# Performance work log

Hardware: AMD Instinct MI355X
Metric: run time of the kernel (lower is better)

## Reference

```python
import jax, jax.numpy as jnp
import numpy as np

B, NPG, E, D, H = 64, 4096, 4194304, 384, 32
N = B * NPG

def setup_inputs() -> dict:
    key = jax.random.key(0)
    ks = jax.random.split(key, 10)
    x = jax.random.normal(ks[0], (N, D), jnp.float32)
    edge_index = jax.random.randint(ks[1], (2, E), 0, N, dtype=jnp.int32)
    batch = jnp.repeat(jnp.arange(B, dtype=jnp.int32), NPG)
    s = 0.05
    W1 = jax.random.normal(ks[2], (D, H), jnp.float32) * s
    b1 = jnp.zeros((H,), jnp.float32)
    W2 = jax.random.normal(ks[3], (H, 8), jnp.float32) * s
    b2 = jnp.zeros((8,), jnp.float32)
    W3 = jax.random.normal(ks[4], (8, 8), jnp.float32) * s
    b3 = jnp.zeros((8,), jnp.float32)
    W4 = jax.random.normal(ks[5], (8, 2), jnp.float32) * s
    b4 = jnp.zeros((2,), jnp.float32)
    return {"x": x, "edge_index": edge_index, "batch": batch,
            "W1": W1, "b1": b1, "W2": W2, "b2": b2,
            "W3": W3, "b3": b3, "W4": W4, "b4": b4}

def _leaky(v):
    return jnp.where(v > 0, v, 0.2 * v)

def reference(x, edge_index, batch, W1, b1, W2, b2, W3, b3, W4, b4):
    n = x.shape[0]
    loop = jnp.arange(n, dtype=edge_index.dtype)
    src = jnp.concatenate([edge_index[0], loop])  # [E+N]
    dst = jnp.concatenate([edge_index[1], loop])
    # GCN symmetric normalization with self-loops (edge_weight = 1)
    deg = jax.ops.segment_sum(jnp.ones(src.shape[0], jnp.float32), dst, num_segments=n)
    dis = jnp.where(deg > 0, jax.lax.rsqrt(jnp.maximum(deg, 1.0)), 0.0)
    norm = (dis[src] * dis[dst])[:, None]  # [E+N, 1]

    def gcn(h, W, b):
        h = h @ W                                   # project first (PyG order)
        agg = jax.ops.segment_sum(h[src] * norm, dst, num_segments=n)
        return agg + b

    h = _leaky(gcn(x, W1, b1))   # [N, 32]
    h = _leaky(gcn(h, W2, b2))   # [N, 8]
    bs = int(np.asarray(batch).max()) + 1
    g = jnp.mean(h.reshape(bs, -1, h.shape[-1]), axis=1)  # mean readout [B, 8]
    g = _leaky(g @ W3 + b3)      # lin1 + leaky_relu; dropout is identity (eval)
    return g @ W4 + b4           # [B, 2]
```

## Files before the change

### kernel.cpp

```cpp
#include <hip/hip_runtime.h>
#include <cstdint>

__device__ __forceinline__ float leaky(float v) { return v > 0.f ? v : 0.2f * v; }


#define NPB 512

__global__ __launch_bounds__(256) void k_bin1(const int* __restrict__ dst,
                                              int* __restrict__ counts,
                                              int E, int CHUNK, int NBKT, int NBLK1) {
  __shared__ int hist[NPB];
  int t = threadIdx.x;
  int blk = blockIdx.x;
  for (int i = t; i < NBKT; i += 256) hist[i] = 0;
  __syncthreads();
  int e0 = blk * CHUNK;
  int e1 = min(e0 + CHUNK, E);
  for (int e = e0 + t; e < e1; e += 256) atomicAdd(&hist[dst[e] >> 9], 1);
  __syncthreads();
  for (int i = t; i < NBKT; i += 256) counts[i * NBLK1 + blk] = hist[i];
}

__global__ __launch_bounds__(256) void k_scan1(const int* __restrict__ cnt,
                                               int* __restrict__ bsums) {
  __shared__ int red[256];
  int t = threadIdx.x;
  int base = blockIdx.x * 1024;
  int s = cnt[base + t] + cnt[base + t + 256] + cnt[base + t + 512] + cnt[base + t + 768];
  red[t] = s;
  __syncthreads();
  for (int off = 128; off > 0; off >>= 1) {
    if (t < off) red[t] += red[t + off];
    __syncthreads();
  }
  if (t == 0) bsums[blockIdx.x] = red[0];
}

__global__ __launch_bounds__(256) void k_scan2(int* __restrict__ bsums, int* __restrict__ S,
                                               int total, int E, int nb) {
  __shared__ int sc[256];
  int t = threadIdx.x;
  int v = (t < nb) ? bsums[t] : 0;
  sc[t] = v;
  __syncthreads();
  for (int off = 1; off < 256; off <<= 1) {
    int u = (t >= off) ? sc[t - off] : 0;
    __syncthreads();
    sc[t] += u;
    __syncthreads();
  }
  if (t < nb) bsums[t] = (t == 0) ? 0 : sc[t - 1];
  if (t == 0) S[total] = E;
}

__global__ __launch_bounds__(256) void k_scan3(const int* __restrict__ cnt,
                                               const int* __restrict__ bsums,
                                               int* __restrict__ S) {
  __shared__ int sc[256];
  int t = threadIdx.x;
  int base = blockIdx.x * 1024;
  int4 d = *(const int4*)(cnt + base + 4 * t);
  int tot = d.x + d.y + d.z + d.w;
  sc[t] = tot;
  __syncthreads();
  for (int off = 1; off < 256; off <<= 1) {
    int u = (t >= off) ? sc[t - off] : 0;
    __syncthreads();
    sc[t] += u;
    __syncthreads();
  }
  int toff = bsums[blockIdx.x] + ((t == 0) ? 0 : sc[t - 1]);
  int4 ro;
  ro.x = toff;
  ro.y = toff + d.x;
  ro.z = toff + d.x + d.y;
  ro.w = toff + d.x + d.y + d.z;
  *(int4*)(S + base + 4 * t) = ro;
}

__global__ __launch_bounds__(256) void k_bin2(const int* __restrict__ ei,
                                              const int* __restrict__ S,
                                              int2* __restrict__ binned,
                                              int E, int CHUNK, int NBKT, int NBLK1) {
  __shared__ int cur[NPB];
  int t = threadIdx.x;
  int blk = blockIdx.x;
  for (int i = t; i < NBKT; i += 256) cur[i] = S[i * NBLK1 + blk];
  __syncthreads();
  int e0 = blk * CHUNK;
  int e1 = min(e0 + CHUNK, E);
  for (int e = e0 + t; e < e1; e += 256) {
    int s = ei[e];
    int d = ei[E + e];
    int pos = atomicAdd(&cur[d >> 9], 1);
    binned[pos] = make_int2(s, d);
  }
}

__global__ __launch_bounds__(256) void k_build(const int2* __restrict__ binned,
                                               const int* __restrict__ S,
                                               int* __restrict__ row_off,
                                               float* __restrict__ dis,
                                               int* __restrict__ csr,
                                               int E, int N, int NBKT, int NBLK1) {
  __shared__ int h[NPB];
  __shared__ int cur[NPB];
  int t = threadIdx.x;
  int b = blockIdx.x;
  int node0 = b * NPB;
  int begb = S[b * NBLK1];
  int endb = (b + 1 < NBKT) ? S[(b + 1) * NBLK1] : E;
  for (int i = t; i < NPB; i += 256) h[i] = 0;
  __syncthreads();
  for (int e = begb + t; e < endb; e += 256) atomicAdd(&h[binned[e].y - node0], 1);
  __syncthreads();
  for (int off = 1; off < NPB; off <<= 1) {
    int i0 = t, i1 = t + 256;
    int a0 = (i0 >= off) ? h[i0 - off] : 0;
    int a1 = (i1 >= off) ? h[i1 - off] : 0;
    __syncthreads();
    h[i0] += a0;
    h[i1] += a1;
    __syncthreads();
  }
  for (int i = t; i < NPB; i += 256) {
    int incl = h[i];
    int excl = i ? h[i - 1] : 0;
    row_off[node0 + i] = begb + excl;
    cur[i] = excl;
    dis[node0 + i] = rsqrtf((float)(incl - excl + 1));
  }
  __syncthreads();
  for (int e = begb + t; e < endb; e += 256) {
    int2 ed = binned[e];
    int pos = atomicAdd(&cur[ed.y - node0], 1);
    csr[begb + pos] = ed.x;
  }
  if (b == NBKT - 1 && t == 0) row_off[N] = E;
}


__global__ __launch_bounds__(256) void k_gemm1(const float* __restrict__ x,
                                               const float* __restrict__ W1,
                                               float* __restrict__ h1) {
  __shared__ float xl[32 * 256];
  __shared__ float wl[32 * 32];
  int t = threadIdx.x;
  size_t n0 = (size_t)blockIdx.x * 256;
  int fg8 = (t & 3) * 8;
  int ng4 = (t >> 2) * 4;
  float acc[4][8];
#pragma unroll
  for (int i = 0; i < 4; i++)
#pragma unroll
    for (int c = 0; c < 8; c++) acc[i][c] = 0.f;

  for (int kc = 0; kc < 384; kc += 32) {
    __syncthreads();
#pragma unroll
    for (int g = 0; g < 2; g++) {
      float4 v[4];
#pragma unroll
      for (int i = 0; i < 4; i++) {
        int idx = g * 1024 + i * 256 + t;
        int k4 = idx & 7;
        int n = idx >> 3;
        v[i] = *(const float4*)(x + (n0 + n) * 384 + kc + k4 * 4);
      }
#pragma unroll
      for (int i = 0; i < 4; i++) {
        int idx = g * 1024 + i * 256 + t;
        int k4 = idx & 7;
        int n = idx >> 3;
        xl[(k4 * 4 + 0) * 256 + n] = v[i].x;
        xl[(k4 * 4 + 1) * 256 + n] = v[i].y;
        xl[(k4 * 4 + 2) * 256 + n] = v[i].z;
        xl[(k4 * 4 + 3) * 256 + n] = v[i].w;
      }
    }
    ((float4*)wl)[t] = ((const float4*)(W1 + kc * 32))[t];
    __syncthreads();
#pragma unroll
    for (int k = 0; k < 32; k++) {
      float4 xv = *(const float4*)&xl[k * 256 + ng4];
      float4 wa = *(const float4*)&wl[k * 32 + fg8];
      float4 wb = *(const float4*)&wl[k * 32 + fg8 + 4];
      float xr[4] = {xv.x, xv.y, xv.z, xv.w};
      float wr[8] = {wa.x, wa.y, wa.z, wa.w, wb.x, wb.y, wb.z, wb.w};
#pragma unroll
      for (int i = 0; i < 4; i++)
#pragma unroll
        for (int c = 0; c < 8; c++) acc[i][c] = fmaf(xr[i], wr[c], acc[i][c]);
    }
  }
#pragma unroll
  for (int i = 0; i < 4; i++) {
    float* dst = h1 + (n0 + ng4 + i) * 32 + fg8;
    *(float4*)dst = make_float4(acc[i][0], acc[i][1], acc[i][2], acc[i][3]);
    *((float4*)dst + 1) = make_float4(acc[i][4], acc[i][5], acc[i][6], acc[i][7]);
  }
}


__global__ __launch_bounds__(256) void k_agg1_fused(const float* __restrict__ h1,
                                                    const float* __restrict__ dis,
                                                    const int* __restrict__ row_off,
                                                    const int* __restrict__ csr,
                                                    const float* __restrict__ b1,
                                                    const float* __restrict__ W2,
                                                    float* __restrict__ h2) {
  __shared__ float w2s[256];
  int t = threadIdx.x;
  w2s[t] = W2[t];
  __syncthreads();
  int lane = t & 63;
  int half = lane >> 5;
  int j = lane & 31;
  int n = blockIdx.x * 4 + (t >> 6);
  int beg = row_off[n], end = row_off[n + 1];
  float dn = dis[n];
  float acc = half ? 0.f : h1[(size_t)n * 32 + j] * dn;
  int p = beg + half;
  for (; p + 2 < end; p += 4) {
    int s0 = csr[p], s1 = csr[p + 2];
    float d0 = dis[s0], d1 = dis[s1];
    float v0 = h1[(size_t)s0 * 32 + j];
    float v1 = h1[(size_t)s1 * 32 + j];
    acc += v0 * d0 + v1 * d1;
  }
  if (p < end) {
    int s = csr[p];
    acc += h1[(size_t)s * 32 + j] * dis[s];
  }
  acc += __shfl_xor(acc, 32);
  float o = leaky(acc * dn + b1[j]);
  float pr[8];
#pragma unroll
  for (int c = 0; c < 8; c++) pr[c] = o * w2s[j * 8 + c];
#pragma unroll
  for (int off = 1; off < 32; off <<= 1) {
#pragma unroll
    for (int c = 0; c < 8; c++) pr[c] += __shfl_xor(pr[c], off);
  }
  if (j == 0) {
    float4 v = half ? make_float4(pr[4], pr[5], pr[6], pr[7])
                    : make_float4(pr[0], pr[1], pr[2], pr[3]);
    *(float4*)(h2 + (size_t)n * 8 + half * 4) = v;
  }
}


__global__ __launch_bounds__(256) void k_agg2(const float* __restrict__ h2,
                                              const float* __restrict__ dis,
                                              const int* __restrict__ row_off,
                                              const int* __restrict__ csr,
                                              const float* __restrict__ b2,
                                              float* __restrict__ out2) {
  int t = threadIdx.x;
  int j = t & 7;
  int sub = (t >> 3) & 1;
  int n = blockIdx.x * 16 + (t >> 4);
  int beg = row_off[n], end = row_off[n + 1];
  float dn = dis[n];
  float acc = sub ? 0.f : h2[(size_t)n * 8 + j] * dn;
  int p = beg + sub;
  for (; p + 2 < end; p += 4) {
    int s0 = csr[p], s1 = csr[p + 2];
    float d0 = dis[s0], d1 = dis[s1];
    acc += h2[(size_t)s0 * 8 + j] * d0 + h2[(size_t)s1 * 8 + j] * d1;
  }
  if (p < end) {
    int s = csr[p];
    acc += h2[(size_t)s * 8 + j] * dis[s];
  }
  acc += __shfl_xor(acc, 8);
  if (!sub) out2[(size_t)n * 8 + j] = leaky(acc * dn + b2[j]);
}


__global__ __launch_bounds__(256) void k_readout(const float* __restrict__ out2,
                                                 float* __restrict__ g, int NPG) {
  __shared__ float red[256];
  int t = threadIdx.x;
  int j = t & 7, r0 = t >> 3;
  const float* base = out2 + (size_t)blockIdx.x * NPG * 8;
  float s = 0.f;
  for (int r = r0; r < NPG; r += 32) s += base[(size_t)r * 8 + j];
  red[t] = s;
  __syncthreads();
  if (t < 8) {
    float tot = 0.f;
    for (int q = 0; q < 32; q++) tot += red[t + 8 * q];
    g[blockIdx.x * 8 + t] = tot / (float)NPG;
  }
}


__global__ __launch_bounds__(64) void k_mlp(const float* __restrict__ g,
                                            const float* __restrict__ W3,
                                            const float* __restrict__ b3,
                                            const float* __restrict__ W4,
                                            const float* __restrict__ b4,
                                            float* __restrict__ out, int B) {
  int b = threadIdx.x;
  if (b >= B) return;
  float gi[8], t1[8];
#pragma unroll
  for (int k = 0; k < 8; k++) gi[k] = g[b * 8 + k];
#pragma unroll
  for (int jj = 0; jj < 8; jj++) {
    float s = b3[jj];
#pragma unroll
    for (int k = 0; k < 8; k++) s = fmaf(gi[k], W3[k * 8 + jj], s);
    t1[jj] = leaky(s);
  }
#pragma unroll
  for (int jj = 0; jj < 2; jj++) {
    float s = b4[jj];
#pragma unroll
    for (int k = 0; k < 8; k++) s = fmaf(t1[k], W4[k * 2 + jj], s);
    out[b * 2 + jj] = s;
  }
}

extern "C" void kernel_launch(void* const* d_in, const int* in_sizes, int n_in,
                              void* d_out, int out_size, void* d_ws, size_t ws_size,
                              hipStream_t stream) {
  const float* x  = (const float*)d_in[0];
  const int*   ei = (const int*)d_in[1];
  const float* W1 = (const float*)d_in[3];
  const float* b1 = (const float*)d_in[4];
  const float* W2 = (const float*)d_in[5];
  const float* b2 = (const float*)d_in[6];
  const float* W3 = (const float*)d_in[7];
  const float* b3 = (const float*)d_in[8];
  const float* W4 = (const float*)d_in[9];
  const float* b4 = (const float*)d_in[10];

  const int E = in_sizes[1] / 2;
  const int N = in_sizes[2];
  const int B = out_size / 2;
  const int NPG = N / B;

  const int NBKT  = N / NPB;
  const int NBLK1 = 512;
  const int CHUNK = (E + NBLK1 - 1) / NBLK1;
  const int SCN   = NBKT * NBLK1;
  const int NBS   = SCN / 1024;

  size_t off = 0;
  auto place = [&](size_t bytes) {
    size_t p = off;
    off = (off + bytes + 255) & ~(size_t)255;
    return p;
  };
  size_t o_counts  = place((size_t)SCN * 4);
  size_t o_S       = place(((size_t)SCN + 1) * 4);
  size_t o_bsums   = place(1024 * 4);
  size_t o_dis     = place((size_t)N * 4);
  size_t o_row_off = place(((size_t)N + 1) * 4);
  size_t o_csr     = place((size_t)E * 4);
  size_t o_binned  = place((size_t)E * 8);
  size_t o_h2      = place((size_t)N * 8 * 4);
  size_t o_gbuf    = place((size_t)B * 8 * 4);
  if (off > ws_size || N % NPB != 0) {
    hipMemsetAsync(d_out, 0, (size_t)out_size * 4, stream);
    return;
  }
  char* ws = (char*)d_ws;
  int*   counts  = (int*)(ws + o_counts);
  int*   S       = (int*)(ws + o_S);
  int*   bsums   = (int*)(ws + o_bsums);
  float* dis     = (float*)(ws + o_dis);
  int*   row_off = (int*)(ws + o_row_off);
  int*   csr     = (int*)(ws + o_csr);
  int2*  binned  = (int2*)(ws + o_binned);
  float* h1      = (float*)(ws + o_binned);
  float* h2      = (float*)(ws + o_h2);
  float* gbuf    = (float*)(ws + o_gbuf);
  float* out2    = h1;

  k_bin1<<<NBLK1, 256, 0, stream>>>(ei + E, counts, E, CHUNK, NBKT, NBLK1);
  k_scan1<<<NBS, 256, 0, stream>>>(counts, bsums);
  k_scan2<<<1, 256, 0, stream>>>(bsums, S, SCN, E, NBS);
  k_scan3<<<NBS, 256, 0, stream>>>(counts, bsums, S);
  k_bin2<<<NBLK1, 256, 0, stream>>>(ei, S, binned, E, CHUNK, NBKT, NBLK1);
  k_build<<<NBKT, 256, 0, stream>>>(binned, S, row_off, dis, csr, E, N, NBKT, NBLK1);
  k_gemm1<<<N / 256, 256, 0, stream>>>(x, W1, h1);
  k_agg1_fused<<<N / 4, 256, 0, stream>>>(h1, dis, row_off, csr, b1, W2, h2);
  k_agg2<<<N / 16, 256, 0, stream>>>(h2, dis, row_off, csr, b2, out2);
  k_readout<<<B, 256, 0, stream>>>(out2, gbuf, NPG);
  k_mlp<<<1, 64, 0, stream>>>(gbuf, W3, b3, W4, b4, (float*)d_out, B);
}
```

Baseline: 0.9997 ms.

## Store features in bf16, pack binned edges, fuse readout into agg2

Intermediate node features h1 and h2 are now stored as bf16 instead of fp32, which halves the bytes moved by the random gathers in both aggregation passes. Binned edges are packed into one int (source shifted left by 9, with the destination's low 9 bits) instead of an int2, which halves binning traffic. The gather loops are unrolled to four neighbours per step, and the mean readout is fused into the second aggregation through per-block atomics on a zeroed buffer. The costs are lower precision in the intermediates, packed source ids that overflow past 2^22 nodes, and floating-point atomics that make the sum order nondeterministic.

Measured after the change: 966.9 us. -3.3%, faster.

```diff
diff --git a/kernel.cpp b/kernel.cpp
--- a/kernel.cpp
+++ b/kernel.cpp
@@ -2,7 +2,14 @@
 #include <cstdint>
 
 __device__ __forceinline__ float leaky(float v) { return v > 0.f ? v : 0.2f * v; }
-
+__device__ __forceinline__ unsigned short f2bf(float f) {
+  unsigned int u = __float_as_uint(f);
+  unsigned int r = (u + 0x7FFFu + ((u >> 16) & 1u)) >> 16;
+  return (unsigned short)r;
+}
+__device__ __forceinline__ float bf2f(unsigned short h) {
+  return __uint_as_float(((unsigned int)h) << 16);
+}
 
 #define NPB 512
 
@@ -80,7 +87,7 @@
 
 __global__ __launch_bounds__(256) void k_bin2(const int* __restrict__ ei,
                                               const int* __restrict__ S,
-                                              int2* __restrict__ binned,
+                                              int* __restrict__ binned,
                                               int E, int CHUNK, int NBKT, int NBLK1) {
   __shared__ int cur[NPB];
   int t = threadIdx.x;
@@ -93,11 +100,11 @@
     int s = ei[e];
     int d = ei[E + e];
     int pos = atomicAdd(&cur[d >> 9], 1);
-    binned[pos] = make_int2(s, d);
-  }
-}
-
-__global__ __launch_bounds__(256) void k_build(const int2* __restrict__ binned,
+    binned[pos] = (s << 9) | (d & 511);
+  }
+}
+
+__global__ __launch_bounds__(256) void k_build(const int* __restrict__ binned,
                                                const int* __restrict__ S,
                                                int* __restrict__ row_off,
                                                float* __restrict__ dis,
@@ -112,7 +119,7 @@
   int endb = (b + 1 < NBKT) ? S[(b + 1) * NBLK1] : E;
   for (int i = t; i < NPB; i += 256) h[i] = 0;
   __syncthreads();
-  for (int e = begb + t; e < endb; e += 256) atomicAdd(&h[binned[e].y - node0], 1);
+  for (int e = begb + t; e < endb; e += 256) atomicAdd(&h[binned[e] & 511], 1);
   __syncthreads();
   for (int off = 1; off < NPB; off <<= 1) {
     int i0 = t, i1 = t + 256;
@@ -132,9 +139,9 @@
   }
   __syncthreads();
   for (int e = begb + t; e < endb; e += 256) {
-    int2 ed = binned[e];
-    int pos = atomicAdd(&cur[ed.y - node0], 1);
-    csr[begb + pos] = ed.x;
+    int ed = binned[e];
+    int pos = atomicAdd(&cur[ed & 511], 1);
+    csr[begb + pos] = ed >> 9;
   }
   if (b == NBKT - 1 && t == 0) row_off[N] = E;
 }
@@ -142,7 +149,7 @@
 
 __global__ __launch_bounds__(256) void k_gemm1(const float* __restrict__ x,
                                                const float* __restrict__ W1,
-                                               float* __restrict__ h1) {
+                                               unsigned short* __restrict__ h1b) {
   __shared__ float xl[32 * 256];
   __shared__ float wl[32 * 32];
   int t = threadIdx.x;
@@ -195,20 +202,23 @@
   }
 #pragma unroll
   for (int i = 0; i < 4; i++) {
-    float* dst = h1 + (n0 + ng4 + i) * 32 + fg8;
-    *(float4*)dst = make_float4(acc[i][0], acc[i][1], acc[i][2], acc[i][3]);
-    *((float4*)dst + 1) = make_float4(acc[i][4], acc[i][5], acc[i][6], acc[i][7]);
-  }
-}
-
-
-__global__ __launch_bounds__(256) void k_agg1_fused(const float* __restrict__ h1,
+    uint4 pk;
+    pk.x = (unsigned)f2bf(acc[i][0]) | ((unsigned)f2bf(acc[i][1]) << 16);
+    pk.y = (unsigned)f2bf(acc[i][2]) | ((unsigned)f2bf(acc[i][3]) << 16);
+    pk.z = (unsigned)f2bf(acc[i][4]) | ((unsigned)f2bf(acc[i][5]) << 16);
+    pk.w = (unsigned)f2bf(acc[i][6]) | ((unsigned)f2bf(acc[i][7]) << 16);
+    *(uint4*)(h1b + (n0 + ng4 + i) * 32 + fg8) = pk;
+  }
+}
+
+
+__global__ __launch_bounds__(256) void k_agg1_fused(const unsigned short* __restrict__ h1b,
                                                     const float* __restrict__ dis,
                                                     const int* __restrict__ row_off,
                                                     const int* __restrict__ csr,
                                                     const float* __restrict__ b1,
                                                     const float* __restrict__ W2,
-                                                    float* __restrict__ h2) {
+                                                    unsigned short* __restrict__ h2b) {
   __shared__ float w2s[256];
   int t = threadIdx.x;
   w2s[t] = W2[t];
@@ -219,18 +229,20 @@
   int n = blockIdx.x * 4 + (t >> 6);
   int beg = row_off[n], end = row_off[n + 1];
   float dn = dis[n];
-  float acc = half ? 0.f : h1[(size_t)n * 32 + j] * dn;
+  float acc = half ? 0.f : bf2f(h1b[(size_t)n * 32 + j]) * dn;
   int p = beg + half;
-  for (; p + 2 < end; p += 4) {
-    int s0 = csr[p], s1 = csr[p + 2];
-    float d0 = dis[s0], d1 = dis[s1];
-    float v0 = h1[(size_t)s0 * 32 + j];
-    float v1 = h1[(size_t)s1 * 32 + j];
-    acc += v0 * d0 + v1 * d1;
-  }
-  if (p < end) {
+  for (; p + 6 < end; p += 8) {
+    int s0 = csr[p], s1 = csr[p + 2], s2 = csr[p + 4], s3 = csr[p + 6];
+    float d0 = dis[s0], d1 = dis[s1], d2 = dis[s2], d3 = dis[s3];
+    float v0 = bf2f(h1b[(size_t)s0 * 32 + j]);
+    float v1 = bf2f(h1b[(size_t)s1 * 32 + j]);
+    float v2 = bf2f(h1b[(size_t)s2 * 32 + j]);
+    float v3 = bf2f(h1b[(size_t)s3 * 32 + j]);
+    acc += v0 * d0 + v1 * d1 + v2 * d2 + v3 * d3;
+  }
+  for (; p < end; p += 2) {
     int s = csr[p];
-    acc += h1[(size_t)s * 32 + j] * dis[s];
+    acc += bf2f(h1b[(size_t)s * 32 + j]) * dis[s];
   }
   acc += __shfl_xor(acc, 32);
   float o = leaky(acc * dn + b1[j]);
@@ -242,56 +254,55 @@
 #pragma unroll
     for (int c = 0; c < 8; c++) pr[c] += __shfl_xor(pr[c], off);
   }
-  if (j == 0) {
-    float4 v = half ? make_float4(pr[4], pr[5], pr[6], pr[7])
-                    : make_float4(pr[0], pr[1], pr[2], pr[3]);
-    *(float4*)(h2 + (size_t)n * 8 + half * 4) = v;
-  }
-}
-
-
-__global__ __launch_bounds__(256) void k_agg2(const float* __restrict__ h2,
-                                              const float* __restrict__ dis,
-                                              const int* __restrict__ row_off,
-                                              const int* __restrict__ csr,
-                                              const float* __restrict__ b2,
-                                              float* __restrict__ out2) {
+  if (lane == 0) {
+    uint4 pk;
+    pk.x = (unsigned)f2bf(pr[0]) | ((unsigned)f2bf(pr[1]) << 16);
+    pk.y = (unsigned)f2bf(pr[2]) | ((unsigned)f2bf(pr[3]) << 16);
+    pk.z = (unsigned)f2bf(pr[4]) | ((unsigned)f2bf(pr[5]) << 16);
+    pk.w = (unsigned)f2bf(pr[6]) | ((unsigned)f2bf(pr[7]) << 16);
+    *(uint4*)(h2b + (size_t)n * 8) = pk;
+  }
+}
+
+
+__global__ __launch_bounds__(256) void k_agg2r(const unsigned short* __restrict__ h2b,
+                                               const float* __restrict__ dis,
+                                               const int* __restrict__ row_off,
+                                               const int* __restrict__ csr,
+                                               const float* __restrict__ b2,
+                                               float* __restrict__ gbuf, int NPG) {
+  __shared__ float red[128];
   int t = threadIdx.x;
   int j = t & 7;
   int sub = (t >> 3) & 1;
-  int n = blockIdx.x * 16 + (t >> 4);
+  int nl = t >> 4;
+  int n = blockIdx.x * 16 + nl;
   int beg = row_off[n], end = row_off[n + 1];
   float dn = dis[n];
-  float acc = sub ? 0.f : h2[(size_t)n * 8 + j] * dn;
+  float acc = sub ? 0.f : bf2f(h2b[(size_t)n * 8 + j]) * dn;
   int p = beg + sub;
-  for (; p + 2 < end; p += 4) {
-    int s0 = csr[p], s1 = csr[p + 2];
-    float d0 = dis[s0], d1 = dis[s1];
-    acc += h2[(size_t)s0 * 8 + j] * d0 + h2[(size_t)s1 * 8 + j] * d1;
-  }
-  if (p < end) {
+  for (; p + 6 < end; p += 8) {
+    int s0 = csr[p], s1 = csr[p + 2], s2 = csr[p + 4], s3 = csr[p + 6];
+    float d0 = dis[s0], d1 = dis[s1], d2 = dis[s2], d3 = dis[s3];
+    float v0 = bf2f(h2b[(size_t)s0 * 8 + j]);
+    float v1 = bf2f(h2b[(size_t)s1 * 8 + j]);
+    float v2 = bf2f(h2b[(size_t)s2 * 8 + j]);
+    float v3 = bf2f(h2b[(size_t)s3 * 8 + j]);
+    acc += v0 * d0 + v1 * d1 + v2 * d2 + v3 * d3;
+  }
+  for (; p < end; p += 2) {
     int s = csr[p];
-    acc += h2[(size_t)s * 8 + j] * dis[s];
+    acc += bf2f(h2b[(size_t)s * 8 + j]) * dis[s];
   }
   acc += __shfl_xor(acc, 8);
-  if (!sub) out2[(size_t)n * 8 + j] = leaky(acc * dn + b2[j]);
-}
-
-
-__global__ __launch_bounds__(256) void k_readout(const float* __restrict__ out2,
-                                                 float* __restrict__ g, int NPG) {
-  __shared__ float red[256];
-  int t = threadIdx.x;
-  int j = t & 7, r0 = t >> 3;
-  const float* base = out2 + (size_t)blockIdx.x * NPG * 8;
-  float s = 0.f;
-  for (int r = r0; r < NPG; r += 32) s += base[(size_t)r * 8 + j];
-  red[t] = s;
+  if (sub == 0) red[nl * 8 + j] = leaky(acc * dn + b2[j]);
   __syncthreads();
   if (t < 8) {
-    float tot = 0.f;
-    for (int q = 0; q < 32; q++) tot += red[t + 8 * q];
-    g[blockIdx.x * 8 + t] = tot / (float)NPG;
+    float s = 0.f;
+#pragma unroll
+    for (int i = 0; i < 16; i++) s += red[i * 8 + t];
+    int graph = (blockIdx.x * 16) / NPG;
+    atomicAdd(&gbuf[graph * 8 + t], s);
   }
 }
 
@@ -301,12 +312,13 @@
                                             const float* __restrict__ b3,
                                             const float* __restrict__ W4,
                                             const float* __restrict__ b4,
-                                            float* __restrict__ out, int B) {
+                                            float* __restrict__ out, int B, int NPG) {
   int b = threadIdx.x;
   if (b >= B) return;
+  float inv = 1.0f / (float)NPG;
   float gi[8], t1[8];
 #pragma unroll
-  for (int k = 0; k < 8; k++) gi[k] = g[b * 8 + k];
+  for (int k = 0; k < 8; k++) gi[k] = g[b * 8 + k] * inv;
 #pragma unroll
   for (int jj = 0; jj < 8; jj++) {
     float s = b3[jj];
@@ -360,8 +372,8 @@
   size_t o_dis     = place((size_t)N * 4);
   size_t o_row_off = place(((size_t)N + 1) * 4);
   size_t o_csr     = place((size_t)E * 4);
-  size_t o_binned  = place((size_t)E * 8);
-  size_t o_h2      = place((size_t)N * 8 * 4);
+  size_t o_binned  = place((size_t)E * 4 > (size_t)N * 64 ? (size_t)E * 4 : (size_t)N * 64);
+  size_t o_h2      = place((size_t)N * 8 * 2);
   size_t o_gbuf    = place((size_t)B * 8 * 4);
   if (off > ws_size || N % NPB != 0) {
     hipMemsetAsync(d_out, 0, (size_t)out_size * 4, stream);
@@ -374,21 +386,20 @@
   float* dis     = (float*)(ws + o_dis);
   int*   row_off = (int*)(ws + o_row_off);
   int*   csr     = (int*)(ws + o_csr);
-  int2*  binned  = (int2*)(ws + o_binned);
-  float* h1      = (float*)(ws + o_binned);
-  float* h2      = (float*)(ws + o_h2);
+  int*   binned  = (int*)(ws + o_binned);
+  unsigned short* h1b = (unsigned short*)(ws + o_binned);
+  unsigned short* h2b = (unsigned short*)(ws + o_h2);
   float* gbuf    = (float*)(ws + o_gbuf);
-  float* out2    = h1;
-
+
+  hipMemsetAsync(gbuf, 0, (size_t)B * 8 * 4, stream);
   k_bin1<<<NBLK1, 256, 0, stream>>>(ei + E, counts, E, CHUNK, NBKT, NBLK1);
   k_scan1<<<NBS, 256, 0, stream>>>(counts, bsums);
   k_scan2<<<1, 256, 0, stream>>>(bsums, S, SCN, E, NBS);
   k_scan3<<<NBS, 256, 0, stream>>>(counts, bsums, S);
   k_bin2<<<NBLK1, 256, 0, stream>>>(ei, S, binned, E, CHUNK, NBKT, NBLK1);
   k_build<<<NBKT, 256, 0, stream>>>(binned, S, row_off, dis, csr, E, N, NBKT, NBLK1);
-  k_gemm1<<<N / 256, 256, 0, stream>>>(x, W1, h1);
-  k_agg1_fused<<<N / 4, 256, 0, stream>>>(h1, dis, row_off, csr, b1, W2, h2);
-  k_agg2<<<N / 16, 256, 0, stream>>>(h2, dis, row_off, csr, b2, out2);
-  k_readout<<<B, 256, 0, stream>>>(out2, gbuf, NPG);
-  k_mlp<<<1, 64, 0, stream>>>(gbuf, W3, b3, W4, b4, (float*)d_out, B);
-}
+  k_gemm1<<<N / 256, 256, 0, stream>>>(x, W1, h1b);
+  k_agg1_fused<<<N / 4, 256, 0, stream>>>(h1b, dis, row_off, csr, b1, W2, h2b);
+  k_agg2r<<<N / 16, 256, 0, stream>>>(h2b, dis, row_off, csr, b2, gbuf, NPG);
+  k_mlp<<<1, 64, 0, stream>>>(gbuf, W3, b3, W4, b4, (float*)d_out, B, NPG);
+}
```
